# Kernel tuning notes

Measured on AMD Instinct MI355X. Metric: run time of the kernel, lower is better.

## Reference

```python
import jax, jax.numpy as jnp
import numpy as np

SS = 25.0 / 255.0   # spatial_scale = 1 / (SEARCH_SIZE/25), SEARCH_SIZE = 255
OUT = 7             # ROIPOOL_OUTSIZE // 4, ROIPOOL_OUTSIZE = 28
SP = 4              # sample_per_part (mmdet DeformRoIPooling default)
TRANS_STD = 0.1


def _deform_roi_pool(x, rois, offset):
    # x: [B,C,H,W]; rois: [N,5] (batch_idx,x1,y1,x2,y2); offset: [N,2,OUT,OUT] (ch0=x, ch1=y)
    B, C, H, W = x.shape
    N = rois.shape[0]
    b = rois[:, 0].astype(jnp.int32)
    sw = jnp.round(rois[:, 1]) * SS - 0.5
    sh = jnp.round(rois[:, 2]) * SS - 0.5
    rw = jnp.maximum((jnp.round(rois[:, 3]) + 1.0) * SS - 0.5 - sw, 0.1)
    rh = jnp.maximum((jnp.round(rois[:, 4]) + 1.0) * SS - 0.5 - sh, 0.1)
    bw, bh = rw / OUT, rh / OUT
    p = jnp.arange(OUT, dtype=x.dtype)
    tx = offset[:, 0] * TRANS_STD  # [N,OUT,OUT] indexed [n,ph,pw]
    ty = offset[:, 1] * TRANS_STD
    wstart = p[None, None, :] * bw[:, None, None] + sw[:, None, None] + tx * rw[:, None, None]
    hstart = p[None, :, None] * bh[:, None, None] + sh[:, None, None] + ty * rh[:, None, None]
    s = jnp.arange(SP, dtype=x.dtype)
    # sample coords [N,OUT,OUT,SP(ih),SP(iw)]
    sx = wstart[..., None, None] + s[None, None, None, None, :] * (bw / SP)[:, None, None, None, None]
    sy = hstart[..., None, None] + s[None, None, None, :, None] * (bh / SP)[:, None, None, None, None]
    valid = (sx >= -0.5) & (sx <= W - 0.5) & (sy >= -0.5) & (sy <= H - 0.5)
    xc = jnp.clip(sx, 0.0, W - 1.0)
    yc = jnp.clip(sy, 0.0, H - 1.0)
    x0 = jnp.floor(xc)
    y0 = jnp.floor(yc)
    dx = xc - x0
    dy = yc - y0
    xi0 = x0.astype(jnp.int32)
    yi0 = y0.astype(jnp.int32)
    xi1 = jnp.ceil(xc).astype(jnp.int32)
    yi1 = jnp.ceil(yc).astype(jnp.int32)
    feat = jnp.transpose(x, (0, 2, 3, 1))  # [B,H,W,C]
    bb = b[:, None, None, None, None]

    def g(yi, xi):
        return feat[bb, yi, xi]  # [N,OUT,OUT,SP,SP,C]

    val = (((1 - dx) * (1 - dy))[..., None] * g(yi0, xi0)
           + (dx * (1 - dy))[..., None] * g(yi0, xi1)
           + ((1 - dx) * dy)[..., None] * g(yi1, xi0)
           + (dx * dy)[..., None] * g(yi1, xi1))
    val = jnp.where(valid[..., None], val, 0.0)
    cnt = valid.sum(axis=(3, 4)).astype(x.dtype)              # [N,OUT,OUT]
    pooled = val.sum(axis=(3, 4)) / jnp.maximum(cnt, 1.0)[..., None]
    return jnp.transpose(pooled, (0, 3, 1, 2))                # [N,C,OUT,OUT]


def _lin(h, w, b):
    return h @ w.T + b


def _forward(x, rois, off_w1, off_b1, off_w2, off_b2, off_w3, off_b3,
             fc1_w, fc1_b, fc2_w, fc2_b, box_w, box_b):
    N = rois.shape[0]
    zero_off = jnp.zeros((N, 2, OUT, OUT), x.dtype)
    # pass 1: no-trans pooling -> offset prediction
    p0 = _deform_roi_pool(x, rois, zero_off).reshape(N, -1)
    h = jax.nn.relu(_lin(p0, off_w1, off_b1))
    h = jax.nn.relu(_lin(h, off_w2, off_b2))
    off = _lin(h, off_w3, off_b3).reshape(N, 2, OUT, OUT)
    # pass 2: deformable pooling with predicted offsets
    p = _deform_roi_pool(x, rois, off).reshape(N, -1)
    h = jax.nn.relu(_lin(p, fc1_w, fc1_b))
    h = jax.nn.relu(_lin(h, fc2_w, fc2_b))
    return _lin(h, box_w, box_b)  # [N,4]


def setup_inputs():
    key = jax.random.key(0)
    ks = jax.random.split(key, 16)
    B, C, H, W, N = 8, 256, 25, 25, 256
    IN = C * OUT * OUT  # 12544
    DFC, FCC = 1024, 512
    x = jax.random.normal(ks[0], (B, C, H, W), jnp.float32)
    bidx = jax.random.randint(ks[1], (N,), 0, B).astype(jnp.float32)
    x1 = jax.random.uniform(ks[2], (N,), minval=0.0, maxval=180.0)
    y1 = jax.random.uniform(ks[3], (N,), minval=0.0, maxval=180.0)
    wd = jax.random.uniform(ks[4], (N,), minval=24.0, maxval=120.0)
    ht = jax.random.uniform(ks[5], (N,), minval=24.0, maxval=120.0)
    rois = jnp.stack([bidx, x1, y1, jnp.clip(x1 + wd, 0.0, 254.0),
                      jnp.clip(y1 + ht, 0.0, 254.0)], axis=1)

    def lin_p(k, o, i):
        return jax.random.normal(k, (o, i), jnp.float32) * (1.0 / np.sqrt(i))

    return dict(
        x=x, rois=rois,
        off_w1=lin_p(ks[6], DFC, IN), off_b1=jnp.zeros((DFC,), jnp.float32),
        off_w2=lin_p(ks[7], DFC, DFC), off_b2=jnp.zeros((DFC,), jnp.float32),
        off_w3=lin_p(ks[8], 2 * OUT * OUT, DFC) * 0.1,
        off_b3=jnp.zeros((2 * OUT * OUT,), jnp.float32),
        fc1_w=lin_p(ks[9], FCC, IN), fc1_b=jnp.zeros((FCC,), jnp.float32),
        fc2_w=lin_p(ks[10], FCC, FCC), fc2_b=jnp.zeros((FCC,), jnp.float32),
        box_w=lin_p(ks[11], 4, FCC) * 0.001, box_b=jnp.zeros((4,), jnp.float32),
    )


def reference(x, rois, off_w1, off_b1, off_w2, off_b2, off_w3, off_b3,
              fc1_w, fc1_b, fc2_w, fc2_b, box_w, box_b):
    return _forward(x, rois, off_w1, off_b1, off_w2, off_b2, off_w3, off_b3,
                    fc1_w, fc1_b, fc2_w, fc2_b, box_w, box_b)
```

## Files before the change

### kernel.cpp

```cpp
#include <hip/hip_runtime.h>
#include <hip/hip_bf16.h>


#define NROI 256
#define CCH  256
#define NB   8
#define INF  12544
#define DFC  1024
#define FCC  512

typedef __attribute__((ext_vector_type(8))) short short8;
typedef __attribute__((ext_vector_type(4))) float floatx4;

static __device__ __forceinline__ unsigned short f2bf(float f) {
    unsigned int u = __float_as_uint(f);
    unsigned int r = (u + 0x7fffu + ((u >> 16) & 1u)) >> 16;
    return (unsigned short)r;
}

__global__ __launch_bounds__(256) void transpose_kernel(
        const float* __restrict__ x, float* __restrict__ xT) {
    __shared__ float t[32][33];
    int b  = blockIdx.z;
    int cb = blockIdx.y * 32;
    int lb = blockIdx.x * 32;
    int tx = threadIdx.x & 31, ty = threadIdx.x >> 5;
#pragma unroll
    for (int r = 0; r < 4; ++r) {
        int c = cb + ty + r * 8, l = lb + tx;
        if (l < 625) t[ty + r * 8][tx] = x[(size_t)(b * 256 + c) * 625 + l];
    }
    __syncthreads();
#pragma unroll
    for (int r = 0; r < 4; ++r) {
        int l = lb + ty + r * 8, c = cb + tx;
        if (l < 625) xT[((size_t)b * 625 + l) * 256 + c] = t[tx][ty + r * 8];
    }
}

__global__ __launch_bounds__(256) void pool_prep(
        const float* __restrict__ rois, const float* __restrict__ off, int has_off,
        float* __restrict__ wbuf, int* __restrict__ bbuf) {
    __shared__ float g[256][16];
    const float SSC = (float)(25.0 / 255.0);
    int tid = threadIdx.x;
    int idx = blockIdx.x * 256 + tid;
    int n = idx / 49;
    int bin = idx - n * 49;
    const float* r = rois + n * 5;
    int b = (int)r[0];
    float sw = rintf(r[1]) * SSC - 0.5f;
    float sh = rintf(r[2]) * SSC - 0.5f;
    float rw = fmaxf((rintf(r[3]) + 1.0f) * SSC - 0.5f - sw, 0.1f);
    float rh = fmaxf((rintf(r[4]) + 1.0f) * SSC - 0.5f - sh, 0.1f);
    float bw = rw / 7.0f, bh = rh / 7.0f;
    float bws = bw * 0.25f, bhs = bh * 0.25f;
    int ph = bin / 7, pw = bin - ph * 7;
    float tx = 0.f, ty = 0.f;
    if (has_off) {
        tx = off[n * 98 + bin] * 0.1f;
        ty = off[n * 98 + 49 + bin] * 0.1f;
    }
    float wstart = pw * bw + sw + tx * rw;
    float hstart = ph * bh + sh + ty * rh;
#pragma unroll
    for (int i = 0; i < 16; ++i) g[tid][i] = 0.f;
    int gy0 = 0, gx0 = 0, cnt = 0;
#pragma unroll
    for (int s = 0; s < 16; ++s) {
        float fx = wstart + (s & 3) * bws;
        float fy = hstart + (s >> 2) * bhs;
        bool valid = (fx >= -0.5f) && (fx <= 24.5f) && (fy >= -0.5f) && (fy <= 24.5f);
        float xc = fminf(fmaxf(fx, 0.f), 24.f);
        float yc = fminf(fmaxf(fy, 0.f), 24.f);
        float x0f = floorf(xc), y0f = floorf(yc);
        float dx = xc - x0f, dy = yc - y0f;
        int x0 = (int)x0f, y0 = (int)y0f;
        int x1 = (int)ceilf(xc), y1 = (int)ceilf(yc);
        if (s == 0) { gy0 = y0; gx0 = x0; }
        float w00 = (1.f - dx) * (1.f - dy), w01 = dx * (1.f - dy);
        float w10 = (1.f - dx) * dy,         w11 = dx * dy;
        if (!valid) { w00 = w01 = w10 = w11 = 0.f; }
        cnt += valid ? 1 : 0;
        int ry0 = (y0 - gy0) * 4, ry1 = (y1 - gy0) * 4;
        g[tid][ry0 + (x0 - gx0)] += w00;
        g[tid][ry0 + (x1 - gx0)] += w01;
        g[tid][ry1 + (x0 - gx0)] += w10;
        g[tid][ry1 + (x1 - gx0)] += w11;
    }
    float inv = 1.0f / fmaxf((float)cnt, 1.0f);
    float4* wp = (float4*)(wbuf + (size_t)idx * 16);
#pragma unroll
    for (int q = 0; q < 4; ++q)
        wp[q] = make_float4(g[tid][q * 4] * inv, g[tid][q * 4 + 1] * inv,
                            g[tid][q * 4 + 2] * inv, g[tid][q * 4 + 3] * inv);
    bbuf[idx] = gy0 | (gx0 << 8) | (b << 16);
}

__global__ __launch_bounds__(256) void pool_gather(
        const float* __restrict__ feat, const float* __restrict__ wbuf,
        const int* __restrict__ bbuf, unsigned short* __restrict__ P,
        float* __restrict__ initDst, const float* __restrict__ initBias, int biasN) {
    __shared__ unsigned short sOut[128 * 49];
    int q = blockIdx.x;
    int n = blockIdx.y;
    int tid = threadIdx.x;
    int wv = tid >> 6, lane = tid & 63;
    int cbase = q * 128 + lane * 2;

    for (int bin = wv; bin < 49; bin += 4) {
        int di = n * 49 + bin;
        int base = bbuf[di];
        int gy0 = base & 255, gx0 = (base >> 8) & 255, b = base >> 16;
        const float4* wp = (const float4*)(wbuf + (size_t)di * 16);
        float4 w0 = wp[0], w1 = wp[1], w2 = wp[2], w3 = wp[3];
        float ww[16] = { w0.x, w0.y, w0.z, w0.w, w1.x, w1.y, w1.z, w1.w,
                         w2.x, w2.y, w2.z, w2.w, w3.x, w3.y, w3.z, w3.w };
        int rowOff[4], colOff[4];
#pragma unroll
        for (int r = 0; r < 4; ++r) {
            rowOff[r] = min(gy0 + r, 24) * 25;
            colOff[r] = min(gx0 + r, 24);
        }
        int b625 = b * 625;
        float ax = 0.f, ay = 0.f;
#pragma unroll
        for (int cell = 0; cell < 16; ++cell) {
            int pix = b625 + rowOff[cell >> 2] + colOff[cell & 3];
            float2 v = *(const float2*)(feat + (size_t)pix * 256 + cbase);
            ax += ww[cell] * v.x;
            ay += ww[cell] * v.y;
        }
        sOut[(lane * 2) * 49 + bin] = f2bf(ax);
        sOut[(lane * 2 + 1) * 49 + bin] = f2bf(ay);
    }
    __syncthreads();
    const uint2* so = (const uint2*)sOut;
    uint2* dp = (uint2*)(P + (size_t)n * INF + q * 128 * 49);
    for (int i = tid; i < 128 * 49 / 4; i += 256) dp[i] = so[i];
    if (q == 0 && initDst)
        for (int i = tid; i < biasN; i += 256)
            initDst[(size_t)n * biasN + i] = initBias[i];
}

template <int BM, int BN>
__global__ __launch_bounds__(256) void gemm_nt_atomic(
        const unsigned short* __restrict__ A, const float* __restrict__ Bw,
        float* __restrict__ C, int M, int N, int K, int kSteps) {
    constexpr int LDA = 40;
    __shared__ unsigned short As[BM * LDA];
    __shared__ unsigned short Bs[BN * LDA];
    const int tid = threadIdx.x;
    const int lane = tid & 63;
    const int wave = tid >> 6;
    const int wm = wave >> 1, wn = wave & 1;
    const int m0 = blockIdx.y * BM;
    const int n0 = blockIdx.x * BN;
    const int k0 = blockIdx.z * kSteps * 32;
    const int quad = lane >> 4;
    const int l16 = lane & 15;
    constexpr int FM = BM / 32, FN = BN / 32;
    constexpr int NA = BM * 4 / 256;
    constexpr int NBq = BN * 8 / 256;

    floatx4 acc[FM][FN];
#pragma unroll
    for (int i = 0; i < FM; ++i)
#pragma unroll
        for (int j = 0; j < FN; ++j) acc[i][j] = (floatx4)0.f;

    uint4  ra[NA];
    float4 rb[NBq];
    auto loadTile = [&](int kk) {
#pragma unroll
        for (int i = 0; i < NA; ++i) {
            int idx = tid + i * 256, row = idx >> 2, qq = idx & 3;
            ra[i] = *(const uint4*)(A + (size_t)(m0 + row) * K + kk + qq * 8);
        }
#pragma unroll
        for (int i = 0; i < NBq; ++i) {
            int idx = tid + i * 256, row = idx >> 3, qq = idx & 7;
            rb[i] = *(const float4*)(Bw + (size_t)(n0 + row) * K + kk + qq * 4);
        }
    };

    loadTile(k0);
    for (int ks = 0; ks < kSteps; ++ks) {
#pragma unroll
        for (int i = 0; i < NA; ++i) {
            int idx = tid + i * 256, row = idx >> 2, qq = idx & 3;
            *(uint4*)(As + row * LDA + qq * 8) = ra[i];
        }
#pragma unroll
        for (int i = 0; i < NBq; ++i) {
            int idx = tid + i * 256, row = idx >> 3, qq = idx & 7;
            ushort4 h;
            h.x = f2bf(rb[i].x); h.y = f2bf(rb[i].y);
            h.z = f2bf(rb[i].z); h.w = f2bf(rb[i].w);
            *(ushort4*)(Bs + row * LDA + qq * 4) = h;
        }
        __syncthreads();
        if (ks + 1 < kSteps) loadTile(k0 + (ks + 1) * 32);
        short8 a[FM], bfr[FN];
#pragma unroll
        for (int i = 0; i < FM; ++i)
            a[i] = *(const short8*)(As + (wm * (BM / 2) + i * 16 + l16) * LDA + quad * 8);
#pragma unroll
        for (int j = 0; j < FN; ++j)
            bfr[j] = *(const short8*)(Bs + (wn * (BN / 2) + j * 16 + l16) * LDA + quad * 8);
#pragma unroll
        for (int i = 0; i < FM; ++i)
#pragma unroll
            for (int j = 0; j < FN; ++j)
                acc[i][j] = __builtin_amdgcn_mfma_f32_16x16x32_bf16(a[i], bfr[j], acc[i][j], 0, 0, 0);
        __syncthreads();
    }
#pragma unroll
    for (int i = 0; i < FM; ++i)
#pragma unroll
        for (int j = 0; j < FN; ++j) {
            int row0 = m0 + wm * (BM / 2) + i * 16 + quad * 4;
            int col = n0 + wn * (BN / 2) + j * 16 + l16;
#pragma unroll
            for (int rr = 0; rr < 4; ++rr)
                atomicAdd(C + (size_t)(row0 + rr) * N + col, acc[i][j][rr]);
        }
}

__global__ __launch_bounds__(256) void relu_cvt_init(
        const float* __restrict__ hin, unsigned short* __restrict__ hbf, int n1,
        float* __restrict__ dst, const float* __restrict__ bias, int biasN, int n2) {
    int idx4 = (blockIdx.x * 256 + threadIdx.x) * 4;
    if (idx4 < n1) {
        float4 v = *(const float4*)(hin + idx4);
        ushort4 h;
        h.x = f2bf(fmaxf(v.x, 0.f)); h.y = f2bf(fmaxf(v.y, 0.f));
        h.z = f2bf(fmaxf(v.z, 0.f)); h.w = f2bf(fmaxf(v.w, 0.f));
        *(ushort4*)(hbf + idx4) = h;
    }
    if (idx4 < n2) {
        int m = biasN - 1;
#pragma unroll
        for (int r = 0; r < 4; ++r) dst[idx4 + r] = bias[(idx4 + r) & m];
    }
}

__global__ __launch_bounds__(128) void fc_small(
        const float* __restrict__ h2, const float* __restrict__ w3,
        const float* __restrict__ b3, float* __restrict__ out) {
    __shared__ float shl[1024];
    int n = blockIdx.x, tid = threadIdx.x;
    for (int i = tid; i < 1024; i += 128) shl[i] = fmaxf(h2[(size_t)n * 1024 + i], 0.f);
    __syncthreads();
    if (tid < 98) {
        float acc = b3[tid];
        const float* w = w3 + (size_t)tid * 1024;
        for (int k = 0; k < 1024; k += 4) {
            float4 wv = *(const float4*)(w + k);
            acc += shl[k] * wv.x + shl[k + 1] * wv.y + shl[k + 2] * wv.z + shl[k + 3] * wv.w;
        }
        out[n * 98 + tid] = acc;
    }
}

__global__ __launch_bounds__(64) void head_kernel(
        const float* __restrict__ h4, const float* __restrict__ bw,
        const float* __restrict__ bb, float* __restrict__ out) {
    int n = blockIdx.x, t = threadIdx.x;
    float a0 = 0, a1 = 0, a2 = 0, a3 = 0;
    for (int k = t; k < 512; k += 64) {
        float v = fmaxf(h4[(size_t)n * 512 + k], 0.f);
        a0 += v * bw[k]; a1 += v * bw[512 + k];
        a2 += v * bw[1024 + k]; a3 += v * bw[1536 + k];
    }
#pragma unroll
    for (int o = 32; o > 0; o >>= 1) {
        a0 += __shfl_down(a0, o); a1 += __shfl_down(a1, o);
        a2 += __shfl_down(a2, o); a3 += __shfl_down(a3, o);
    }
    if (t == 0) {
        out[n * 4 + 0] = a0 + bb[0]; out[n * 4 + 1] = a1 + bb[1];
        out[n * 4 + 2] = a2 + bb[2]; out[n * 4 + 3] = a3 + bb[3];
    }
}

extern "C" void kernel_launch(void* const* d_in, const int* in_sizes, int n_in,
                              void* d_out, int out_size, void* d_ws, size_t ws_size,
                              hipStream_t stream) {
    const float* x      = (const float*)d_in[0];
    const float* rois   = (const float*)d_in[1];
    const float* off_w1 = (const float*)d_in[2];
    const float* off_b1 = (const float*)d_in[3];
    const float* off_w2 = (const float*)d_in[4];
    const float* off_b2 = (const float*)d_in[5];
    const float* off_w3 = (const float*)d_in[6];
    const float* off_b3 = (const float*)d_in[7];
    const float* fc1_w  = (const float*)d_in[8];
    const float* fc1_b  = (const float*)d_in[9];
    const float* fc2_w  = (const float*)d_in[10];
    const float* fc2_b  = (const float*)d_in[11];
    const float* box_w  = (const float*)d_in[12];
    const float* box_b  = (const float*)d_in[13];
    float* out = (float*)d_out;

    char* ws = (char*)d_ws;
    size_t o = 0;
    auto carve = [&](size_t bytes) { char* p = ws + o; o += (bytes + 255) & ~(size_t)255; return p; };
    float*          xT   = (float*)carve((size_t)NB * 625 * 256 * 4);
    unsigned short* p0   = (unsigned short*)carve((size_t)NROI * INF * 2);
    unsigned short* p1   = (unsigned short*)carve((size_t)NROI * INF * 2);
    float*          h1   = (float*)carve((size_t)NROI * DFC * 4);
    unsigned short* h1b  = (unsigned short*)carve((size_t)NROI * DFC * 2);
    float*          h2   = (float*)carve((size_t)NROI * DFC * 4);
    float*          offb = (float*)carve((size_t)NROI * 98 * 4);
    float*          h3   = (float*)carve((size_t)NROI * FCC * 4);
    unsigned short* h3b  = (unsigned short*)carve((size_t)NROI * FCC * 2);
    float*          h4   = (float*)carve((size_t)NROI * FCC * 4);
    float*          wbuf = (float*)carve((size_t)NROI * 49 * 16 * 4);
    int*            bbuf = (int*)carve((size_t)NROI * 49 * 4);

    transpose_kernel<<<dim3(20, 8, 8), 256, 0, stream>>>(x, xT);
    pool_prep<<<49, 256, 0, stream>>>(rois, nullptr, 0, wbuf, bbuf);
    pool_gather<<<dim3(2, NROI), 256, 0, stream>>>(xT, wbuf, bbuf, p0, h1, off_b1, DFC);
    gemm_nt_atomic<128, 64><<<dim3(16, 2, 28), 256, 0, stream>>>(p0, off_w1, h1, NROI, DFC, INF, 14);
    relu_cvt_init<<<256, 256, 0, stream>>>(h1, h1b, NROI * DFC, h2, off_b2, DFC, NROI * DFC);
    gemm_nt_atomic<128, 64><<<dim3(16, 2, 16), 256, 0, stream>>>(h1b, off_w2, h2, NROI, DFC, DFC, 2);
    fc_small<<<NROI, 128, 0, stream>>>(h2, off_w3, off_b3, offb);
    pool_prep<<<49, 256, 0, stream>>>(rois, offb, 1, wbuf, bbuf);
    pool_gather<<<dim3(2, NROI), 256, 0, stream>>>(xT, wbuf, bbuf, p1, h3, fc1_b, FCC);
    gemm_nt_atomic<128, 64><<<dim3(8, 2, 49), 256, 0, stream>>>(p1, fc1_w, h3, NROI, FCC, INF, 8);
    relu_cvt_init<<<128, 256, 0, stream>>>(h3, h3b, NROI * FCC, h4, fc2_b, FCC, NROI * FCC);
    gemm_nt_atomic<64, 64><<<dim3(8, 4, 8), 256, 0, stream>>>(h3b, fc2_w, h4, NROI, FCC, FCC, 2);
    head_kernel<<<NROI, 64, 0, stream>>>(h4, box_w, box_b, out);
}
```

Baseline: 351.9 us.

## Replace atomic split-K accumulation with partial slabs and fused reduce-bias-relu kernels

Split-K GEMMs now write per-slice partial results to a workspace slab instead of issuing float atomicAdds, and a new reduce kernel sums the partials, adds bias, applies ReLU and converts to bf16 in one pass. This removes the bias-init step in pool_gather and the separate relu/convert kernels. Tile shapes are changed to BN=32 and the split count adapts to available workspace. It adds extra global memory traffic for the partial slabs (up to 28 slabs of 1 MB each) in exchange for avoiding atomic contention.

Result: slower. 394.6 us (+12.1%).

```diff
diff --git a/kernel.cpp b/kernel.cpp
--- a/kernel.cpp
+++ b/kernel.cpp
@@ -3,7 +3,6 @@
 
 
 #define NROI 256
-#define CCH  256
 #define NB   8
 #define INF  12544
 #define DFC  1024
@@ -99,8 +98,7 @@
 
 __global__ __launch_bounds__(256) void pool_gather(
         const float* __restrict__ feat, const float* __restrict__ wbuf,
-        const int* __restrict__ bbuf, unsigned short* __restrict__ P,
-        float* __restrict__ initDst, const float* __restrict__ initBias, int biasN) {
+        const int* __restrict__ bbuf, unsigned short* __restrict__ P) {
     __shared__ unsigned short sOut[128 * 49];
     int q = blockIdx.x;
     int n = blockIdx.y;
@@ -138,15 +136,12 @@
     const uint2* so = (const uint2*)sOut;
     uint2* dp = (uint2*)(P + (size_t)n * INF + q * 128 * 49);
     for (int i = tid; i < 128 * 49 / 4; i += 256) dp[i] = so[i];
-    if (q == 0 && initDst)
-        for (int i = tid; i < biasN; i += 256)
-            initDst[(size_t)n * biasN + i] = initBias[i];
 }
 
 template <int BM, int BN>
-__global__ __launch_bounds__(256) void gemm_nt_atomic(
+__global__ __launch_bounds__(256) void gemm_nt_part(
         const unsigned short* __restrict__ A, const float* __restrict__ Bw,
-        float* __restrict__ C, int M, int N, int K, int kSteps) {
+        float* __restrict__ Cpart, int M, int N, int K, int kSteps) {
     constexpr int LDA = 40;
     __shared__ unsigned short As[BM * LDA];
     __shared__ unsigned short Bs[BN * LDA];
@@ -215,6 +210,7 @@
                 acc[i][j] = __builtin_amdgcn_mfma_f32_16x16x32_bf16(a[i], bfr[j], acc[i][j], 0, 0, 0);
         __syncthreads();
     }
+    float* Cp = Cpart + (size_t)blockIdx.z * M * N;
 #pragma unroll
     for (int i = 0; i < FM; ++i)
 #pragma unroll
@@ -223,26 +219,34 @@
             int col = n0 + wn * (BN / 2) + j * 16 + l16;
 #pragma unroll
             for (int rr = 0; rr < 4; ++rr)
-                atomicAdd(C + (size_t)(row0 + rr) * N + col, acc[i][j][rr]);
-        }
-}
-
-__global__ __launch_bounds__(256) void relu_cvt_init(
-        const float* __restrict__ hin, unsigned short* __restrict__ hbf, int n1,
-        float* __restrict__ dst, const float* __restrict__ bias, int biasN, int n2) {
-    int idx4 = (blockIdx.x * 256 + threadIdx.x) * 4;
-    if (idx4 < n1) {
-        float4 v = *(const float4*)(hin + idx4);
+                Cp[(size_t)(row0 + rr) * N + col] = acc[i][j][rr];
+        }
+}
+
+__global__ __launch_bounds__(256) void reduce_bias(
+        const float* __restrict__ part, int zc, int mn4,
+        const float* __restrict__ bias, int nmask, int relu,
+        unsigned short* __restrict__ obf, float* __restrict__ of) {
+    int idx = blockIdx.x * 256 + threadIdx.x;
+    if (idx >= mn4) return;
+    int idx4 = idx * 4;
+    const float* bp = bias + (idx4 & nmask);
+    float4 acc = *(const float4*)bp;
+    const float4* p = (const float4*)part + idx;
+    for (int z = 0; z < zc; ++z) {
+        float4 v = p[(size_t)z * mn4];
+        acc.x += v.x; acc.y += v.y; acc.z += v.z; acc.w += v.w;
+    }
+    if (relu) {
+        acc.x = fmaxf(acc.x, 0.f); acc.y = fmaxf(acc.y, 0.f);
+        acc.z = fmaxf(acc.z, 0.f); acc.w = fmaxf(acc.w, 0.f);
+    }
+    if (obf) {
         ushort4 h;
-        h.x = f2bf(fmaxf(v.x, 0.f)); h.y = f2bf(fmaxf(v.y, 0.f));
-        h.z = f2bf(fmaxf(v.z, 0.f)); h.w = f2bf(fmaxf(v.w, 0.f));
-        *(ushort4*)(hbf + idx4) = h;
-    }
-    if (idx4 < n2) {
-        int m = biasN - 1;
-#pragma unroll
-        for (int r = 0; r < 4; ++r) dst[idx4 + r] = bias[(idx4 + r) & m];
-    }
+        h.x = f2bf(acc.x); h.y = f2bf(acc.y); h.z = f2bf(acc.z); h.w = f2bf(acc.w);
+        *(ushort4*)(obf + idx4) = h;
+    }
+    if (of) *(float4*)(of + idx4) = acc;
 }
 
 __global__ __launch_bounds__(128) void fc_small(
@@ -307,29 +311,38 @@
     size_t o = 0;
     auto carve = [&](size_t bytes) { char* p = ws + o; o += (bytes + 255) & ~(size_t)255; return p; };
     float*          xT   = (float*)carve((size_t)NB * 625 * 256 * 4);
-    unsigned short* p0   = (unsigned short*)carve((size_t)NROI * INF * 2);
-    unsigned short* p1   = (unsigned short*)carve((size_t)NROI * INF * 2);
-    float*          h1   = (float*)carve((size_t)NROI * DFC * 4);
+    unsigned short* P    = (unsigned short*)carve((size_t)NROI * INF * 2);
     unsigned short* h1b  = (unsigned short*)carve((size_t)NROI * DFC * 2);
     float*          h2   = (float*)carve((size_t)NROI * DFC * 4);
     float*          offb = (float*)carve((size_t)NROI * 98 * 4);
-    float*          h3   = (float*)carve((size_t)NROI * FCC * 4);
     unsigned short* h3b  = (unsigned short*)carve((size_t)NROI * FCC * 2);
     float*          h4   = (float*)carve((size_t)NROI * FCC * 4);
     float*          wbuf = (float*)carve((size_t)NROI * 49 * 16 * 4);
     int*            bbuf = (int*)carve((size_t)NROI * 49 * 4);
+    size_t fixed = o;
+    const size_t SLAB = (size_t)NROI * DFC * 4;
+    int zg1;
+    if      (ws_size >= fixed + 28 * SLAB) zg1 = 28;
+    else if (ws_size >= fixed + 14 * SLAB) zg1 = 14;
+    else if (ws_size >= fixed +  7 * SLAB) zg1 = 7;
+    else                                   zg1 = 4;
+    int zg4 = zg1 * 2;
+    int zg2 = (zg1 >= 14) ? 8 : 4;
+    float* part = (float*)carve((size_t)zg1 * SLAB);
 
     transpose_kernel<<<dim3(20, 8, 8), 256, 0, stream>>>(x, xT);
     pool_prep<<<49, 256, 0, stream>>>(rois, nullptr, 0, wbuf, bbuf);
-    pool_gather<<<dim3(2, NROI), 256, 0, stream>>>(xT, wbuf, bbuf, p0, h1, off_b1, DFC);
-    gemm_nt_atomic<128, 64><<<dim3(16, 2, 28), 256, 0, stream>>>(p0, off_w1, h1, NROI, DFC, INF, 14);
-    relu_cvt_init<<<256, 256, 0, stream>>>(h1, h1b, NROI * DFC, h2, off_b2, DFC, NROI * DFC);
-    gemm_nt_atomic<128, 64><<<dim3(16, 2, 16), 256, 0, stream>>>(h1b, off_w2, h2, NROI, DFC, DFC, 2);
+    pool_gather<<<dim3(2, NROI), 256, 0, stream>>>(xT, wbuf, bbuf, P);
+    gemm_nt_part<128, 32><<<dim3(32, 2, zg1), 256, 0, stream>>>(P, off_w1, part, NROI, DFC, INF, 392 / zg1);
+    reduce_bias<<<256, 256, 0, stream>>>(part, zg1, NROI * DFC / 4, off_b1, DFC - 1, 1, h1b, nullptr);
+    gemm_nt_part<128, 32><<<dim3(32, 2, zg2), 256, 0, stream>>>(h1b, off_w2, part, NROI, DFC, DFC, 32 / zg2);
+    reduce_bias<<<256, 256, 0, stream>>>(part, zg2, NROI * DFC / 4, off_b2, DFC - 1, 0, nullptr, h2);
     fc_small<<<NROI, 128, 0, stream>>>(h2, off_w3, off_b3, offb);
     pool_prep<<<49, 256, 0, stream>>>(rois, offb, 1, wbuf, bbuf);
-    pool_gather<<<dim3(2, NROI), 256, 0, stream>>>(xT, wbuf, bbuf, p1, h3, fc1_b, FCC);
-    gemm_nt_atomic<128, 64><<<dim3(8, 2, 49), 256, 0, stream>>>(p1, fc1_w, h3, NROI, FCC, INF, 8);
-    relu_cvt_init<<<128, 256, 0, stream>>>(h3, h3b, NROI * FCC, h4, fc2_b, FCC, NROI * FCC);
-    gemm_nt_atomic<64, 64><<<dim3(8, 4, 8), 256, 0, stream>>>(h3b, fc2_w, h4, NROI, FCC, FCC, 2);
+    pool_gather<<<dim3(2, NROI), 256, 0, stream>>>(xT, wbuf, bbuf, P);
+    gemm_nt_part<128, 32><<<dim3(16, 2, zg4), 256, 0, stream>>>(P, fc1_w, part, NROI, FCC, INF, 392 / zg4);
+    reduce_bias<<<128, 256, 0, stream>>>(part, zg4, NROI * FCC / 4, fc1_b, FCC - 1, 1, h3b, nullptr);
+    gemm_nt_part<64, 32><<<dim3(16, 4, 4), 256, 0, stream>>>(h3b, fc2_w, part, NROI, FCC, FCC, 4);
+    reduce_bias<<<128, 256, 0, stream>>>(part, 4, NROI * FCC / 4, fc2_b, FCC - 1, 0, nullptr, h4);
     head_kernel<<<NROI, 64, 0, stream>>>(h4, box_w, box_b, out);
 }
```
